# Kernel tuning notes

Measured on AMD Instinct MI355X. Metric: run time of the kernel, lower is better.

Reference implementation:

```python
import jax, jax.numpy as jnp
import numpy as np

D_MODEL = 1024
N_HEADS = 16
DH = D_MODEL // N_HEADS
ROPE_THETA = 10000.0


def rotate_half(u):
    h = u.shape[-1] // 2
    return jnp.concatenate([-u[..., h:], u[..., :h]], axis=-1)


def apply_rope(q, k, cos, sin):
    return q * cos + rotate_half(q) * sin, k * cos + rotate_half(k) * sin


def setup_inputs() -> dict:
    key = jax.random.key(0)
    ks = jax.random.split(key, 6)
    B, S = 2, 2048
    x = jax.random.normal(ks[0], (B, S, D_MODEL), dtype=jnp.float32)
    y = jax.random.normal(ks[1], (B, S, D_MODEL), dtype=jnp.float32)
    wq = 0.01 * jax.random.normal(ks[2], (D_MODEL, D_MODEL), dtype=jnp.float32)
    wk = 0.01 * jax.random.normal(ks[3], (D_MODEL, D_MODEL), dtype=jnp.float32)
    wv = 0.01 * jax.random.normal(ks[4], (D_MODEL, D_MODEL), dtype=jnp.float32)
    wo = 0.01 * jax.random.normal(ks[5], (D_MODEL, D_MODEL), dtype=jnp.float32)
    return {"x": x, "y": y, "wq": wq, "wk": wk, "wv": wv, "wo": wo}


def reference(x, y, wq, wk, wv, wo):
    B, S, D = x.shape
    past_length = 0  # default; kv_cache=None

    Q = x @ wq.T                      # (B,S,D)
    K = y                             # NOTE: K is y un-projected (as in source)
    V = y @ wv.T
    # K1 = x @ wk.T is computed in the source but immediately overwritten
    # by the buggy second apply_rope call -> wk is unused in the output.
    V1 = x @ wo.T

    def heads(t):
        return t.reshape(B, S, N_HEADS, DH).transpose(0, 2, 1, 3)  # (B,H,S,dh)

    q_h, k_h, v_h, v1_h = heads(Q), heads(K), heads(V), heads(V1)

    # RoPE tables (past_length:past_length+S rows of the cache)
    freqs = 1.0 / ROPE_THETA ** (jnp.arange(0, DH, 2, dtype=jnp.float32) / DH)
    emb = jnp.arange(past_length, past_length + S, dtype=jnp.float32)[:, None] * freqs[None, :]
    cos = jnp.concatenate([jnp.cos(emb), jnp.cos(emb)], axis=-1)[None, None]  # (1,1,S,dh)
    sin = jnp.concatenate([jnp.sin(emb), jnp.sin(emb)], axis=-1)[None, None]

    q_h, k_h = apply_rope(q_h, k_h, cos, sin)
    # faithful to source: k1 = rope applied AGAIN to the already-roped k
    _, k1_h = apply_rope(q_h, k_h, cos, sin)

    k_full = jnp.concatenate([k_h, k1_h], axis=2)   # (B,H,2S,dh)
    v_full = jnp.concatenate([v_h, v1_h], axis=2)
    S_full = k_full.shape[2]

    # mask: tril(diagonal=past_length) over (S,S_full), last S cols = eye(S)
    rows = jnp.arange(S)[:, None]
    cols = jnp.arange(S_full)[None, :]
    mask = cols <= rows + past_length
    mask = mask.at[:, -S:].set(jnp.eye(S, dtype=bool))  # (S,S_full)

    scores = jnp.einsum("bhqd,bhkd->bhqk", q_h, k_full) / jnp.sqrt(jnp.asarray(DH, x.dtype))
    scores = jnp.where(mask[None, None], scores, jnp.asarray(-1e30, x.dtype))
    attn = jax.nn.softmax(scores, axis=-1)
    out = jnp.einsum("bhqk,bhkd->bhqd", attn, v_full)
    out = out.transpose(0, 2, 1, 3).reshape(B, S, D)

    k_ret = k_full[:, :, :-S, :]
    return out, k_ret
```

## Files before the change

kernel.cpp:

```cpp
#include <hip/hip_runtime.h>

#define DM 1024
#define NHEADS 16
#define DHEAD 64
#define BB 2
#define SS 2048
#define BH (BB*NHEADS)

typedef __attribute__((ext_vector_type(8))) short short8;
typedef __attribute__((ext_vector_type(4))) short short4v;
typedef __attribute__((ext_vector_type(4))) float float4v;
typedef unsigned short ushort_t;

#define LN1E4_D32 0.28782313662425572f
#define SM_SCALE  0.18033688011112042f

static __device__ __forceinline__ unsigned short f2bf(float f) {
    union { float f; unsigned u; } v; v.f = f;
    unsigned r = v.u + 0x7fffu + ((v.u >> 16) & 1u);
    return (unsigned short)(r >> 16);
}
static __device__ __forceinline__ float bf2f(unsigned short u) {
    union { float f; unsigned u; } v; v.u = ((unsigned)u) << 16;
    return v.f;
}
static __device__ __forceinline__ unsigned cvtpk_bf16(float lo, float hi) {
    unsigned r;
    asm("v_cvt_pk_bf16_f32 %0, %1, %2" : "=v"(r) : "v"(lo), "v"(hi));
    return r;
}
static __device__ __forceinline__ float ex2(float x) {
    float r;
    asm("v_exp_f32 %0, %1" : "=v"(r) : "v"(x));
    return r;
}
static __device__ __forceinline__ short4v lo4(short8 v) {
    return __builtin_shufflevector(v, v, 0, 1, 2, 3);
}
static __device__ __forceinline__ short4v hi4(short8 v) {
    return __builtin_shufflevector(v, v, 4, 5, 6, 7);
}

static __device__ __forceinline__ void gload16(const ushort_t* g, ushort_t* l) {
    __builtin_amdgcn_global_load_lds(
        (const __attribute__((address_space(1))) void*)g,
        (__attribute__((address_space(3))) void*)l, 16, 0, 0);
}

__global__ __launch_bounds__(256) void prep_kernel(
        const float* __restrict__ x, const float* __restrict__ y,
        const float* __restrict__ wq, const float* __restrict__ wv,
        const float* __restrict__ wo,
        ushort_t* __restrict__ xb, ushort_t* __restrict__ wqb,
        ushort_t* __restrict__ wvb, ushort_t* __restrict__ wob,
        float* __restrict__ kout, ushort_t* __restrict__ khb,
        ushort_t* __restrict__ yb) {
    if (blockIdx.x < 3584) {
        int C = blockIdx.x * 256 + threadIdx.x;
        int c  = C & 511;
        int tl = C >> 9;
        int rb = tl >> 5, kb = tl & 31;
        const float* src; ushort_t* dst; int r0;
        if (rb < 32)      { src = x;  r0 = rb * 128;        dst = xb  + (size_t)tl * 4096; }
        else if (rb < 40) { src = wq; r0 = (rb - 32) * 128; dst = wqb + (size_t)(((rb - 32) * 32) + kb) * 4096; }
        else if (rb < 48) { src = wv; r0 = (rb - 40) * 128; dst = wvb + (size_t)(((rb - 40) * 32) + kb) * 4096; }
        else              { src = wo; r0 = (rb - 48) * 128; dst = wob + (size_t)(((rb - 48) * 32) + kb) * 4096; }
        int row = c >> 2, g = c & 3;
        int kk3 = g ^ ((row >> 1) & 3);
        const float* s = src + (size_t)(r0 + row) * DM + kb * 32 + kk3 * 8;
        float4 a0 = *reinterpret_cast<const float4*>(s);
        float4 a1 = *reinterpret_cast<const float4*>(s + 4);
        short8 v;
        v[0] = (short)f2bf(a0.x); v[1] = (short)f2bf(a0.y);
        v[2] = (short)f2bf(a0.z); v[3] = (short)f2bf(a0.w);
        v[4] = (short)f2bf(a1.x); v[5] = (short)f2bf(a1.y);
        v[6] = (short)f2bf(a1.z); v[7] = (short)f2bf(a1.w);
        *reinterpret_cast<short8*>(dst + c * 8) = v;
        return;
    }
    int t = (blockIdx.x - 3584) * 256 + threadIdx.x;
    int i8 = t & 3;
    int s  = (t >> 2) & (SS - 1);
    int bh = t >> 13;
    int h = bh & (NHEADS - 1), b = bh >> 4;

    const float* yp = y + ((size_t)(b * SS + s)) * DM + h * DHEAD + i8 * 8;
    float4 a0 = *reinterpret_cast<const float4*>(yp);
    float4 a1 = *reinterpret_cast<const float4*>(yp + 4);
    float4 b0 = *reinterpret_cast<const float4*>(yp + 32);
    float4 b1 = *reinterpret_cast<const float4*>(yp + 36);
    float u0[8] = {a0.x, a0.y, a0.z, a0.w, a1.x, a1.y, a1.z, a1.w};
    float u1[8] = {b0.x, b0.y, b0.z, b0.w, b1.x, b1.y, b1.z, b1.w};
    float lo[8], hi[8];
#pragma unroll
    for (int j = 0; j < 8; j++) {
        int i = i8 * 8 + j;
        float freq = __expf(-(float)i * LN1E4_D32);
        float th = (float)s * freq;
        float cv, sv;
        __sincosf(th, &sv, &cv);
        lo[j] = u0[j] * cv - u1[j] * sv;
        hi[j] = u1[j] * cv + u0[j] * sv;
    }
    float* op = kout + ((size_t)bh * SS + s) * DHEAD + i8 * 8;
    *reinterpret_cast<float4*>(op)      = (float4){lo[0], lo[1], lo[2], lo[3]};
    *reinterpret_cast<float4*>(op + 4)  = (float4){lo[4], lo[5], lo[6], lo[7]};
    *reinterpret_cast<float4*>(op + 32) = (float4){hi[0], hi[1], hi[2], hi[3]};
    *reinterpret_cast<float4*>(op + 36) = (float4){hi[4], hi[5], hi[6], hi[7]};

    ushort_t* kb = khb + ((size_t)bh * 32 + (s >> 6)) * 4096 + (s & 63) * 64;
    short8 vlo, vhi;
#pragma unroll
    for (int j = 0; j < 8; j++) { vlo[j] = (short)f2bf(lo[j]); vhi[j] = (short)f2bf(hi[j]); }
    *reinterpret_cast<short8*>(kb + ((i8 ^ (s & 7)) << 3))       = vlo;
    *reinterpret_cast<short8*>(kb + (((i8 + 4) ^ (s & 7)) << 3)) = vhi;

    int rowm = b * SS + s;
    int rowin = rowm & 127, rbm = rowm >> 7;
    int g = i8 ^ ((rowin >> 1) & 3);
    ushort_t* yt = yb + ((size_t)(rbm * 32 + h * 2)) * 4096 + rowin * 32 + (g << 3);
    short8 ulo, uhi;
#pragma unroll
    for (int j = 0; j < 8; j++) { ulo[j] = (short)f2bf(u0[j]); uhi[j] = (short)f2bf(u1[j]); }
    *reinterpret_cast<short8*>(yt)        = ulo;
    *reinterpret_cast<short8*>(yt + 4096) = uhi;
}

__global__ __launch_bounds__(256, 2) void gemm3_kernel(
        const ushort_t* __restrict__ xb, const ushort_t* __restrict__ yb,
        const ushort_t* __restrict__ wqb, const ushort_t* __restrict__ wvb,
        const ushort_t* __restrict__ wob,
        ushort_t* __restrict__ qh, ushort_t* __restrict__ vt, ushort_t* __restrict__ v1h) {
    __shared__ __align__(16) char smem[49152];
    ushort_t* As = (ushort_t*)smem;
    ushort_t* Bs = (ushort_t*)(smem + 16384);
    ushort_t* Cs = (ushort_t*)(smem + 32768);
    ushort_t (*Ct)[136] = (ushort_t(*)[136])smem;

    int bid = blockIdx.x;
    int xcd = bid & 7;
    int s_  = bid >> 3;
    int merged = (s_ < 32);
    int t_  = s_ & 31;
    int n0  = (t_ >> 2) * 128;
    int m0  = (xcd * 4 + (t_ & 3)) * 128;

    const ushort_t* A  = merged ? xb : yb;
    const ushort_t* W1 = merged ? wqb : wvb;

    const ushort_t* Atl = A   + (size_t)(m0 >> 7) * 32 * 4096;
    const ushort_t* W1t = W1  + (size_t)(n0 >> 7) * 32 * 4096;
    const ushort_t* W2t = wob + (size_t)(n0 >> 7) * 32 * 4096;

    int tid = threadIdx.x;
    int wave = tid >> 6, lane = tid & 63, quad = lane >> 4, l15 = lane & 15;
    int wr = (wave >> 1) * 64, wc = (wave & 1) * 64;

    int gi0 = tid * 8, gi1 = (256 + tid) * 8;
    int li0 = (tid & 192) * 8, li1 = (256 + (tid & 192)) * 8;

    int aoff[4], boff[4];
#pragma unroll
    for (int mi = 0; mi < 4; mi++) {
        int row = wr + mi * 16 + l15;
        aoff[mi] = row * 32 + ((quad ^ ((row >> 1) & 3)) << 3);
    }
#pragma unroll
    for (int ni = 0; ni < 4; ni++) {
        int row = wc + ni * 16 + l15;
        boff[ni] = row * 32 + ((quad ^ ((row >> 1) & 3)) << 3);
    }

    float4v acc1[4][4], acc2[4][4];
#pragma unroll
    for (int a = 0; a < 4; a++)
#pragma unroll
        for (int b = 0; b < 4; b++) {
            acc1[a][b] = (float4v){0.f, 0.f, 0.f, 0.f};
            acc2[a][b] = (float4v){0.f, 0.f, 0.f, 0.f};
        }

    gload16(Atl + gi0, As + li0); gload16(Atl + gi1, As + li1);
    gload16(W1t + gi0, Bs + li0); gload16(W1t + gi1, Bs + li1);
    if (merged) { gload16(W2t + gi0, Cs + li0); gload16(W2t + gi1, Cs + li1); }
    int cur = 0;

    for (int kb = 0; kb < 32; kb++) {
        __syncthreads();
        if (kb + 1 < 32) {
            const ushort_t* at = Atl + (size_t)(kb + 1) * 4096;
            const ushort_t* w1 = W1t + (size_t)(kb + 1) * 4096;
            int nb = (cur ^ 1) * 4096;
            gload16(at + gi0, As + nb + li0); gload16(at + gi1, As + nb + li1);
            gload16(w1 + gi0, Bs + nb + li0); gload16(w1 + gi1, Bs + nb + li1);
            if (merged) {
                const ushort_t* w2 = W2t + (size_t)(kb + 1) * 4096;
                gload16(w2 + gi0, Cs + nb + li0); gload16(w2 + gi1, Cs + nb + li1);
            }
        }
        const ushort_t* Ac = As + cur * 4096;
        const ushort_t* Bc = Bs + cur * 4096;
        const ushort_t* Cc = Cs + cur * 4096;
        short8 af[4], b1[4];
#pragma unroll
        for (int mi = 0; mi < 4; mi++)
            af[mi] = *reinterpret_cast<const short8*>(&Ac[aoff[mi]]);
#pragma unroll
        for (int ni = 0; ni < 4; ni++)
            b1[ni] = *reinterpret_cast<const short8*>(&Bc[boff[ni]]);
#pragma unroll
        for (int mi = 0; mi < 4; mi++)
#pragma unroll
            for (int ni = 0; ni < 4; ni++)
                acc1[mi][ni] = __builtin_amdgcn_mfma_f32_16x16x32_bf16(af[mi], b1[ni], acc1[mi][ni], 0, 0, 0);
        if (merged) {
            short8 b2[4];
#pragma unroll
            for (int ni = 0; ni < 4; ni++)
                b2[ni] = *reinterpret_cast<const short8*>(&Cc[boff[ni]]);
#pragma unroll
            for (int mi = 0; mi < 4; mi++)
#pragma unroll
                for (int ni = 0; ni < 4; ni++)
                    acc2[mi][ni] = __builtin_amdgcn_mfma_f32_16x16x32_bf16(af[mi], b2[ni], acc2[mi][ni], 0, 0, 0);
        }
        cur ^= 1;
    }

    int h0 = n0 >> 6;
    if (merged) {
#pragma unroll
        for (int mi = 0; mi < 4; mi++)
#pragma unroll
            for (int r = 0; r < 4; r++) {
                int m = m0 + wr + mi * 16 + quad * 4 + r;
                float pos = (float)(m & (SS - 1));
#pragma unroll
                for (int ni = 0; ni < 2; ni++) {
                    int d = ni * 16 + l15;
                    float f = __expf(-(float)d * LN1E4_D32);
                    float th = pos * f;
                    float cv, sv;
                    __sincosf(th, &sv, &cv);
                    cv *= SM_SCALE; sv *= SM_SCALE;
                    float u0 = acc1[mi][ni][r], u1 = acc1[mi][ni + 2][r];
                    acc1[mi][ni][r]     = u0 * cv - u1 * sv;
                    acc1[mi][ni + 2][r] = u1 * cv + u0 * sv;
                }
            }
        __syncthreads();
#pragma unroll
        for (int mi = 0; mi < 4; mi++)
#pragma unroll
            for (int ni = 0; ni < 4; ni++) {
                int col = wc + ni * 16 + l15;
#pragma unroll
                for (int r = 0; r < 4; r++)
                    Ct[wr + mi * 16 + quad * 4 + r][col] = f2bf(acc1[mi][ni][r]);
            }
        __syncthreads();
#pragma unroll
        for (int it = 0; it < 8; it++) {
            int c = it * 256 + tid;
            int o = c >> 3, j = c & 7;
            int hh = o >> 7, mr = o & 127;
            int m = m0 + mr, b = m >> 11, si = m & (SS - 1);
            uint4 v = *reinterpret_cast<const uint4*>(&Ct[mr][hh * 64 + j * 8]);
            *reinterpret_cast<uint4*>(
                &qh[((size_t)((b * NHEADS + h0 + hh) * SS + si)) * DHEAD + j * 8]) = v;
        }
        __syncthreads();
#pragma unroll
        for (int mi = 0; mi < 4; mi++)
#pragma unroll
            for (int ni = 0; ni < 4; ni++) {
                int col = wc + ni * 16 + l15;
#pragma unroll
                for (int r = 0; r < 4; r++)
                    Ct[wr + mi * 16 + quad * 4 + r][col] = f2bf(acc2[mi][ni][r]);
            }
        __syncthreads();
#pragma unroll
        for (int it = 0; it < 8; it++) {
            int c = it * 256 + tid;
            int o = c >> 3, j = c & 7;
            int hh = o >> 7, mr = o & 127;
            int m = m0 + mr, b = m >> 11, si = m & (SS - 1);
            uint4 v = *reinterpret_cast<const uint4*>(&Ct[mr][hh * 64 + j * 8]);
            *reinterpret_cast<uint4*>(
                &v1h[((size_t)((b * NHEADS + h0 + hh) * SS + si)) * DHEAD + j * 8]) = v;
        }
    } else {
        __syncthreads();
#pragma unroll
        for (int mi = 0; mi < 4; mi++)
#pragma unroll
            for (int ni = 0; ni < 4; ni++) {
                int col = wc + ni * 16 + l15;
#pragma unroll
                for (int r = 0; r < 4; r++)
                    Ct[wr + mi * 16 + quad * 4 + r][col] = f2bf(acc1[mi][ni][r]);
            }
        __syncthreads();
        int b = m0 >> 11;
        int s0 = m0 & (SS - 1);
#pragma unroll
        for (int it = 0; it < 8; it++) {
            int c = it * 256 + tid;
            int dh6 = c & 63;
            int rest = c >> 6;
            int hh = rest >> 4;
            int th = (rest >> 3) & 1;
            int cq = rest & 7;
            int q = cq >> 1, sHalf = cq & 1;
            short8 v;
#pragma unroll
            for (int e = 0; e < 8; e++) {
                int t2 = 2 * sHalf + (e >> 2), j = e & 3;
                int kw = 16 * t2 + 4 * q + j;
                v[e] = (short)Ct[th * 64 + kw][hh * 64 + dh6];
            }
            int kt = (s0 >> 6) + th;
            size_t off = ((size_t)((b * NHEADS + h0 + hh) * 32 + kt)) * 4096
                       + dh6 * 64 + ((cq ^ (dh6 & 7)) << 3);
            *reinterpret_cast<short8*>(&vt[off]) = v;
        }
    }
}

template<bool MASKED>
static __device__ __forceinline__ void attn_tile(
        const ushort_t* __restrict__ Kc, const ushort_t* __restrict__ Vc, int kbase,
        int quad, int l15, int q0w, const short8* qf, const short4v& ones4,
        float4v* Oa, float4v& sum4) {
    float4v sa[4];
#pragma unroll
    for (int t2 = 0; t2 < 4; t2++) sa[t2] = (float4v){0.f, 0.f, 0.f, 0.f};
    __builtin_amdgcn_s_setprio(1);
#pragma unroll
    for (int t2 = 0; t2 < 4; t2++) {
        int key = t2 * 16 + l15;
        int ro = key * 64, sw = key & 7;
#pragma unroll
        for (int half = 0; half < 2; half++) {
            short8 kf = *reinterpret_cast<const short8*>(&Kc[ro + (((half * 4 + quad) ^ sw) << 3)]);
            sa[t2] = __builtin_amdgcn_mfma_f32_16x16x32_bf16(kf, qf[half], sa[t2], 0, 0, 0);
        }
    }
    __builtin_amdgcn_s_setprio(0);
    int query = q0w + l15;
    short4v pa[4];
#pragma unroll
    for (int t2 = 0; t2 < 4; t2++) {
        float p[4];
#pragma unroll
        for (int r = 0; r < 4; r++) {
            float e = ex2(sa[t2][r]);
            if (MASKED) {
                int key = kbase + t2 * 16 + quad * 4 + r;
                p[r] = (key <= query) ? e : 0.f;
            } else {
                p[r] = e;
            }
        }
        union { short4v s; unsigned u[2]; } pu;
        pu.u[0] = cvtpk_bf16(p[0], p[1]);
        pu.u[1] = cvtpk_bf16(p[2], p[3]);
        pa[t2] = pu.s;
    }
    __builtin_amdgcn_s_setprio(1);
#pragma unroll
    for (int t2 = 0; t2 < 4; t2++)
        sum4 = __builtin_amdgcn_mfma_f32_16x16x16bf16_1k(pa[t2], ones4, sum4, 0, 0, 0);
#pragma unroll
    for (int t = 0; t < 4; t++) {
        int dh = t * 16 + l15;
        int ro = dh * 64, sw = dh & 7;
        short8 v0 = *reinterpret_cast<const short8*>(&Vc[ro + (((quad * 2 + 0) ^ sw) << 3)]);
        short8 v1 = *reinterpret_cast<const short8*>(&Vc[ro + (((quad * 2 + 1) ^ sw) << 3)]);
        Oa[t] = __builtin_amdgcn_mfma_f32_16x16x16bf16_1k(pa[0], lo4(v0), Oa[t], 0, 0, 0);
        Oa[t] = __builtin_amdgcn_mfma_f32_16x16x16bf16_1k(pa[1], hi4(v0), Oa[t], 0, 0, 0);
        Oa[t] = __builtin_amdgcn_mfma_f32_16x16x16bf16_1k(pa[2], lo4(v1), Oa[t], 0, 0, 0);
        Oa[t] = __builtin_amdgcn_mfma_f32_16x16x16bf16_1k(pa[3], hi4(v1), Oa[t], 0, 0, 0);
    }
    __builtin_amdgcn_s_setprio(0);
}

__global__ __launch_bounds__(512, 4) void attn_kernel(
        const ushort_t* __restrict__ qh, const float* __restrict__ kf32,
        const ushort_t* __restrict__ khb, const ushort_t* __restrict__ vtb,
        const ushort_t* __restrict__ v1h, float* __restrict__ out) {
    __shared__ __align__(16) ushort_t Ks[4][4096];
    __shared__ __align__(16) ushort_t Vt[4][4096];
    __shared__ float sdiag_s[8][16];

    int bid = blockIdx.x;
    int bh = (bid & 7) * 4 + ((bid >> 3) & 3);
    int p  = bid >> 5;

    int tid = threadIdx.x, wave = tid >> 6, lane = tid & 63, quad = lane >> 4, l15 = lane & 15;
    int jq  = (wave < 4) ? p : (31 - p);
    int q0w = jq * 64 + (wave & 3) * 16;
    const ushort_t* qp  = qh  + (size_t)bh * SS * DHEAD;
    const float*    kp  = kf32 + (size_t)bh * SS * DHEAD;
    const ushort_t* v1p = v1h + (size_t)bh * SS * DHEAD;
    const ushort_t* ktb = khb + (size_t)bh * 32 * 4096;
    const ushort_t* vtt = vtb + (size_t)bh * 32 * 4096;

    short8 qf[2];
    qf[0] = *reinterpret_cast<const short8*>(&qp[(q0w + l15) * DHEAD + quad * 8]);
    qf[1] = *reinterpret_cast<const short8*>(&qp[(q0w + l15) * DHEAD + 32 + quad * 8]);
    short4v ones4;
#pragma unroll
    for (int j = 0; j < 4; j++) ones4[j] = (short)0x3F80;

    float4v Oa[4];
#pragma unroll
    for (int t = 0; t < 4; t++) Oa[t] = (float4v){0.f, 0.f, 0.f, 0.f};
    float4v sum4 = (float4v){0.f, 0.f, 0.f, 0.f};

    int gi = tid * 8;
    int li = (tid & 448) * 8;

    int ntiles = 32 - p;
    gload16(ktb + gi, &Ks[0][li]);               gload16(vtt + gi, &Vt[0][li]);
    gload16(ktb + 4096 + gi, &Ks[1][li]);        gload16(vtt + 4096 + gi, &Vt[1][li]);

    int kt = 0;
    for (; kt + 1 < ntiles; kt += 2) {
        __syncthreads();
        if (kt + 2 < ntiles) {
            const ushort_t* gk = ktb + (size_t)(kt + 2) * 4096;
            const ushort_t* gv = vtt + (size_t)(kt + 2) * 4096;
            int nb = (kt + 2) & 3;
            gload16(gk + gi, &Ks[nb][li]);
            gload16(gv + gi, &Vt[nb][li]);
        }
        if (kt + 3 < ntiles) {
            const ushort_t* gk = ktb + (size_t)(kt + 3) * 4096;
            const ushort_t* gv = vtt + (size_t)(kt + 3) * 4096;
            int nb = (kt + 3) & 3;
            gload16(gk + gi, &Ks[nb][li]);
            gload16(gv + gi, &Vt[nb][li]);
        }
        {
            int kbase = kt * 64, sl = kt & 3;
            if (kbase <= q0w + 15) {
                if (kbase + 63 <= q0w)
                    attn_tile<false>(Ks[sl], Vt[sl], kbase, quad, l15, q0w, qf, ones4, Oa, sum4);
                else
                    attn_tile<true>(Ks[sl], Vt[sl], kbase, quad, l15, q0w, qf, ones4, Oa, sum4);
            }
        }
        {
            int kbase = (kt + 1) * 64, sl = (kt + 1) & 3;
            if (kbase <= q0w + 15) {
                if (kbase + 63 <= q0w)
                    attn_tile<false>(Ks[sl], Vt[sl], kbase, quad, l15, q0w, qf, ones4, Oa, sum4);
                else
                    attn_tile<true>(Ks[sl], Vt[sl], kbase, quad, l15, q0w, qf, ones4, Oa, sum4);
            }
        }
    }
    if (kt < ntiles) {
        __syncthreads();
        int kbase = kt * 64, sl = kt & 3;
        if (kbase <= q0w + 15) {
            if (kbase + 63 <= q0w)
                attn_tile<false>(Ks[sl], Vt[sl], kbase, quad, l15, q0w, qf, ones4, Oa, sum4);
            else
                attn_tile<true>(Ks[sl], Vt[sl], kbase, quad, l15, q0w, qf, ones4, Oa, sum4);
        }
    }

    float* sdiag = sdiag_s[wave];

    {
        int sk = q0w + l15;
        const float* krow = kp + (size_t)sk * DHEAD;
        short8 k1lo, k1hi;
#pragma unroll
        for (int j = 0; j < 8; j++) {
            int d = quad * 8 + j;
            float f = __expf(-(float)d * LN1E4_D32);
            float th = (float)sk * f;
            float cv, sv;
            __sincosf(th, &sv, &cv);
            float a = krow[d], b2 = krow[d + 32];
            k1lo[j] = (short)f2bf(a * cv - b2 * sv);
            k1hi[j] = (short)f2bf(b2 * cv + a * sv);
        }
        float4v sd4 = (float4v){0.f, 0.f, 0.f, 0.f};
        sd4 = __builtin_amdgcn_mfma_f32_16x16x32_bf16(qf[0], k1lo, sd4, 0, 0, 0);
        sd4 = __builtin_amdgcn_mfma_f32_16x16x32_bf16(qf[1], k1hi, sd4, 0, 0, 0);
#pragma unroll
        for (int r = 0; r < 4; r++)
            if (l15 == quad * 4 + r) sdiag[l15] = sd4[r];

        int b = bh >> 4, h = bh & (NHEADS - 1);
#pragma unroll
        for (int r = 0; r < 4; r++) {
            float pd = ex2(sdiag[quad * 4 + r]);
            int query = q0w + quad * 4 + r;
            float linv = 1.f / (sum4[r] + pd);
#pragma unroll
            for (int t = 0; t < 4; t++) {
                float v1v = bf2f(v1p[query * DHEAD + t * 16 + l15]);
                float o = (Oa[t][r] + pd * v1v) * linv;
                out[(b * SS + query) * DM + h * DHEAD + t * 16 + l15] = o;
            }
        }
    }
}

extern "C" void kernel_launch(void* const* d_in, const int* in_sizes, int n_in,
                              void* d_out, int out_size, void* d_ws, size_t ws_size,
                              hipStream_t stream) {
    const float* x  = (const float*)d_in[0];
    const float* y  = (const float*)d_in[1];
    const float* wq = (const float*)d_in[2];
    const float* wv = (const float*)d_in[4];
    const float* wo = (const float*)d_in[5];
    float* outp  = (float*)d_out;
    float* k_out = outp + (size_t)BB * SS * DM;

    char* ws = (char*)d_ws;
    ushort_t* vtb = (ushort_t*)(ws);
    ushort_t* v1b = (ushort_t*)(ws + (8ull  << 20));
    ushort_t* qhb = (ushort_t*)(ws + (16ull << 20));
    ushort_t* khb = (ushort_t*)(ws + (24ull << 20));
    ushort_t* xb  = (ushort_t*)(ws + (32ull << 20));
    ushort_t* yb  = (ushort_t*)(ws + (40ull << 20));
    ushort_t* wqb = (ushort_t*)(ws + (48ull << 20));
    ushort_t* wvb = (ushort_t*)(ws + (50ull << 20));
    ushort_t* wob = (ushort_t*)(ws + (52ull << 20));

    prep_kernel<<<4608, 256, 0, stream>>>(x, y, wq, wv, wo, xb, wqb, wvb, wob,
                                          k_out, khb, yb);
    gemm3_kernel<<<512, 256, 0, stream>>>(xb, yb, wqb, wvb, wob, qhb, vtb, v1b);
    attn_kernel<<<512, 512, 0, stream>>>(qhb, k_out, khb, vtb, v1b, outp);
}
```

Measured before the change: 164.3 us.

## Load attention K/V fragments straight into registers, dropping LDS staging and barriers

The producer kernels now write K and V^T tiles in a fragment-major layout, so each lane's MFMA operand is one contiguous 16-byte chunk. The attention kernel stops staging shared K/V tiles in LDS with block-wide barriers. Each wave loads its own fragments from global memory into registers, double-buffered (A/B) so the next tile's loads overlap the current tile's MFMAs. Each wave now loops only over the tiles its own queries need, rather than the whole block's tile range. In exchange, K/V reuse across the 8 waves now relies on cache instead of LDS, register pressure rises, and launch bounds drop from 4 to 2 blocks per CU.

```diff
diff --git a/kernel.cpp b/kernel.cpp
--- a/kernel.cpp
+++ b/kernel.cpp
@@ -108,12 +108,12 @@
     *reinterpret_cast<float4*>(op + 32) = (float4){hi[0], hi[1], hi[2], hi[3]};
     *reinterpret_cast<float4*>(op + 36) = (float4){hi[4], hi[5], hi[6], hi[7]};
 
-    ushort_t* kb = khb + ((size_t)bh * 32 + (s >> 6)) * 4096 + (s & 63) * 64;
+    ushort_t* kb = khb + ((size_t)bh * 32 + (s >> 6)) * 4096;
     short8 vlo, vhi;
 #pragma unroll
     for (int j = 0; j < 8; j++) { vlo[j] = (short)f2bf(lo[j]); vhi[j] = (short)f2bf(hi[j]); }
-    *reinterpret_cast<short8*>(kb + ((i8 ^ (s & 7)) << 3))       = vlo;
-    *reinterpret_cast<short8*>(kb + (((i8 + 4) ^ (s & 7)) << 3)) = vhi;
+    *reinterpret_cast<short8*>(kb + ((i8       * 64 + (s & 63)) << 3)) = vlo;
+    *reinterpret_cast<short8*>(kb + (((i8 + 4) * 64 + (s & 63)) << 3)) = vhi;
 
     int rowm = b * SS + s;
     int rowin = rowm & 127, rbm = rowm >> 7;
@@ -322,15 +322,32 @@
             }
             int kt = (s0 >> 6) + th;
             size_t off = ((size_t)((b * NHEADS + h0 + hh) * 32 + kt)) * 4096
-                       + dh6 * 64 + ((cq ^ (dh6 & 7)) << 3);
+                       + ((cq * 64 + dh6) << 3);
             *reinterpret_cast<short8*>(&vt[off]) = v;
         }
     }
 }
 
+static __device__ __forceinline__ void load_tile(
+        const ushort_t* __restrict__ Kt, const ushort_t* __restrict__ Vt,
+        int quad, int l15, short8 kf[4][2], short8 vf[4][2]) {
+#pragma unroll
+    for (int t2 = 0; t2 < 4; t2++)
+#pragma unroll
+        for (int half = 0; half < 2; half++)
+            kf[t2][half] = *reinterpret_cast<const short8*>(
+                &Kt[(((half * 4 + quad) * 64 + t2 * 16 + l15)) << 3]);
+#pragma unroll
+    for (int t = 0; t < 4; t++)
+#pragma unroll
+        for (int s = 0; s < 2; s++)
+            vf[t][s] = *reinterpret_cast<const short8*>(
+                &Vt[(((quad * 2 + s) * 64 + t * 16 + l15)) << 3]);
+}
+
 template<bool MASKED>
-static __device__ __forceinline__ void attn_tile(
-        const ushort_t* __restrict__ Kc, const ushort_t* __restrict__ Vc, int kbase,
+static __device__ __forceinline__ void compute_tile(
+        const short8 kf[4][2], const short8 vf[4][2], int kbase,
         int quad, int l15, int q0w, const short8* qf, const short4v& ones4,
         float4v* Oa, float4v& sum4) {
     float4v sa[4];
@@ -338,15 +355,10 @@
     for (int t2 = 0; t2 < 4; t2++) sa[t2] = (float4v){0.f, 0.f, 0.f, 0.f};
     __builtin_amdgcn_s_setprio(1);
 #pragma unroll
-    for (int t2 = 0; t2 < 4; t2++) {
-        int key = t2 * 16 + l15;
-        int ro = key * 64, sw = key & 7;
-#pragma unroll
-        for (int half = 0; half < 2; half++) {
-            short8 kf = *reinterpret_cast<const short8*>(&Kc[ro + (((half * 4 + quad) ^ sw) << 3)]);
-            sa[t2] = __builtin_amdgcn_mfma_f32_16x16x32_bf16(kf, qf[half], sa[t2], 0, 0, 0);
-        }
-    }
+    for (int t2 = 0; t2 < 4; t2++)
+#pragma unroll
+        for (int half = 0; half < 2; half++)
+            sa[t2] = __builtin_amdgcn_mfma_f32_16x16x32_bf16(kf[t2][half], qf[half], sa[t2], 0, 0, 0);
     __builtin_amdgcn_s_setprio(0);
     int query = q0w + l15;
     short4v pa[4];
@@ -374,24 +386,18 @@
         sum4 = __builtin_amdgcn_mfma_f32_16x16x16bf16_1k(pa[t2], ones4, sum4, 0, 0, 0);
 #pragma unroll
     for (int t = 0; t < 4; t++) {
-        int dh = t * 16 + l15;
-        int ro = dh * 64, sw = dh & 7;
-        short8 v0 = *reinterpret_cast<const short8*>(&Vc[ro + (((quad * 2 + 0) ^ sw) << 3)]);
-        short8 v1 = *reinterpret_cast<const short8*>(&Vc[ro + (((quad * 2 + 1) ^ sw) << 3)]);
-        Oa[t] = __builtin_amdgcn_mfma_f32_16x16x16bf16_1k(pa[0], lo4(v0), Oa[t], 0, 0, 0);
-        Oa[t] = __builtin_amdgcn_mfma_f32_16x16x16bf16_1k(pa[1], hi4(v0), Oa[t], 0, 0, 0);
-        Oa[t] = __builtin_amdgcn_mfma_f32_16x16x16bf16_1k(pa[2], lo4(v1), Oa[t], 0, 0, 0);
-        Oa[t] = __builtin_amdgcn_mfma_f32_16x16x16bf16_1k(pa[3], hi4(v1), Oa[t], 0, 0, 0);
+        Oa[t] = __builtin_amdgcn_mfma_f32_16x16x16bf16_1k(pa[0], lo4(vf[t][0]), Oa[t], 0, 0, 0);
+        Oa[t] = __builtin_amdgcn_mfma_f32_16x16x16bf16_1k(pa[1], hi4(vf[t][0]), Oa[t], 0, 0, 0);
+        Oa[t] = __builtin_amdgcn_mfma_f32_16x16x16bf16_1k(pa[2], lo4(vf[t][1]), Oa[t], 0, 0, 0);
+        Oa[t] = __builtin_amdgcn_mfma_f32_16x16x16bf16_1k(pa[3], hi4(vf[t][1]), Oa[t], 0, 0, 0);
     }
     __builtin_amdgcn_s_setprio(0);
 }
 
-__global__ __launch_bounds__(512, 4) void attn_kernel(
+__global__ __launch_bounds__(512, 2) void attn_kernel(
         const ushort_t* __restrict__ qh, const float* __restrict__ kf32,
         const ushort_t* __restrict__ khb, const ushort_t* __restrict__ vtb,
         const ushort_t* __restrict__ v1h, float* __restrict__ out) {
-    __shared__ __align__(16) ushort_t Ks[4][4096];
-    __shared__ __align__(16) ushort_t Vt[4][4096];
     __shared__ float sdiag_s[8][16];
 
     int bid = blockIdx.x;
@@ -419,58 +425,26 @@
     for (int t = 0; t < 4; t++) Oa[t] = (float4v){0.f, 0.f, 0.f, 0.f};
     float4v sum4 = (float4v){0.f, 0.f, 0.f, 0.f};
 
-    int gi = tid * 8;
-    int li = (tid & 448) * 8;
-
-    int ntiles = 32 - p;
-    gload16(ktb + gi, &Ks[0][li]);               gload16(vtt + gi, &Vt[0][li]);
-    gload16(ktb + 4096 + gi, &Ks[1][li]);        gload16(vtt + 4096 + gi, &Vt[1][li]);
-
+    short8 kA[4][2], vA[4][2], kB[4][2], vB[4][2];
+
+    if (jq > 0) load_tile(ktb, vtt, quad, l15, kA, vA);
     int kt = 0;
-    for (; kt + 1 < ntiles; kt += 2) {
-        __syncthreads();
-        if (kt + 2 < ntiles) {
-            const ushort_t* gk = ktb + (size_t)(kt + 2) * 4096;
-            const ushort_t* gv = vtt + (size_t)(kt + 2) * 4096;
-            int nb = (kt + 2) & 3;
-            gload16(gk + gi, &Ks[nb][li]);
-            gload16(gv + gi, &Vt[nb][li]);
-        }
-        if (kt + 3 < ntiles) {
-            const ushort_t* gk = ktb + (size_t)(kt + 3) * 4096;
-            const ushort_t* gv = vtt + (size_t)(kt + 3) * 4096;
-            int nb = (kt + 3) & 3;
-            gload16(gk + gi, &Ks[nb][li]);
-            gload16(gv + gi, &Vt[nb][li]);
-        }
-        {
-            int kbase = kt * 64, sl = kt & 3;
-            if (kbase <= q0w + 15) {
-                if (kbase + 63 <= q0w)
-                    attn_tile<false>(Ks[sl], Vt[sl], kbase, quad, l15, q0w, qf, ones4, Oa, sum4);
-                else
-                    attn_tile<true>(Ks[sl], Vt[sl], kbase, quad, l15, q0w, qf, ones4, Oa, sum4);
-            }
-        }
-        {
-            int kbase = (kt + 1) * 64, sl = (kt + 1) & 3;
-            if (kbase <= q0w + 15) {
-                if (kbase + 63 <= q0w)
-                    attn_tile<false>(Ks[sl], Vt[sl], kbase, quad, l15, q0w, qf, ones4, Oa, sum4);
-                else
-                    attn_tile<true>(Ks[sl], Vt[sl], kbase, quad, l15, q0w, qf, ones4, Oa, sum4);
-            }
-        }
-    }
-    if (kt < ntiles) {
-        __syncthreads();
-        int kbase = kt * 64, sl = kt & 3;
-        if (kbase <= q0w + 15) {
-            if (kbase + 63 <= q0w)
-                attn_tile<false>(Ks[sl], Vt[sl], kbase, quad, l15, q0w, qf, ones4, Oa, sum4);
-            else
-                attn_tile<true>(Ks[sl], Vt[sl], kbase, quad, l15, q0w, qf, ones4, Oa, sum4);
-        }
+    for (; kt + 1 < jq; kt += 2) {
+        load_tile(ktb + (size_t)(kt + 1) * 4096, vtt + (size_t)(kt + 1) * 4096,
+                  quad, l15, kB, vB);
+        compute_tile<false>(kA, vA, kt * 64, quad, l15, q0w, qf, ones4, Oa, sum4);
+        if (kt + 2 < jq)
+            load_tile(ktb + (size_t)(kt + 2) * 4096, vtt + (size_t)(kt + 2) * 4096,
+                      quad, l15, kA, vA);
+        compute_tile<false>(kB, vB, (kt + 1) * 64, quad, l15, q0w, qf, ones4, Oa, sum4);
+    }
+    if (kt < jq) {
+        load_tile(ktb + (size_t)jq * 4096, vtt + (size_t)jq * 4096, quad, l15, kB, vB);
+        compute_tile<false>(kA, vA, kt * 64, quad, l15, q0w, qf, ones4, Oa, sum4);
+        compute_tile<true>(kB, vB, jq * 64, quad, l15, q0w, qf, ones4, Oa, sum4);
+    } else {
+        load_tile(ktb + (size_t)jq * 4096, vtt + (size_t)jq * 4096, quad, l15, kA, vA);
+        compute_tile<true>(kA, vA, jq * 64, quad, l15, q0w, qf, ones4, Oa, sum4);
     }
 
     float* sdiag = sdiag_s[wave];
```

Result: slower. 178.7 us (+8.8%).
